# Kernel optimization log

Hardware: AMD Instinct MI355X
Metric: run time of the kernel (lower is better)

The kernel has to match this reference:

```python
import jax, jax.numpy as jnp
import numpy as np

EMBED_DIM = 1408
NUM_HEADS = 16
HEAD_DIM = EMBED_DIM // NUM_HEADS  # 88
SCALE = HEAD_DIM ** -0.5


def setup_inputs() -> dict:
    key = jax.random.key(0)
    k0, k1, k2, k3, k4 = jax.random.split(key, 5)
    B, S, D = 16, 577, EMBED_DIM
    hidden_states = jax.random.normal(k0, (B, S, D), dtype=jnp.float32)
    # fused QKV projection: [D, 3D] laid out as [q | k | v]
    w_qkv = jax.random.normal(k1, (D, 3 * D), dtype=jnp.float32) * (D ** -0.5)
    b_qkv = jax.random.normal(k2, (3 * D,), dtype=jnp.float32) * 0.02
    # output projection
    w_proj = jax.random.normal(k3, (D, D), dtype=jnp.float32) * (D ** -0.5)
    b_proj = jax.random.normal(k4, (D,), dtype=jnp.float32) * 0.02
    return {
        "hidden_states": hidden_states,
        "w_qkv": w_qkv,
        "b_qkv": b_qkv,
        "w_proj": w_proj,
        "b_proj": b_proj,
    }


def reference(hidden_states, w_qkv, b_qkv, w_proj, b_proj):
    B, S, D = hidden_states.shape
    H, Hd = NUM_HEADS, HEAD_DIM
    # fused QKV projection, then chunk along last dim (matches .chunk(3, -1))
    qkv = hidden_states @ w_qkv + b_qkv                      # [B, S, 3D]
    q, k, v = jnp.split(qkv, 3, axis=-1)                     # each [B, S, D]
    q = q.reshape(B, S, H, Hd)
    k = k.reshape(B, S, H, Hd)
    v = v.reshape(B, S, H, Hd)
    # scaled dot-product attention (no mask, no dropout at inference)
    scores = jnp.einsum("bqhd,bkhd->bhqk", q, k) * SCALE      # [B, H, S, S]
    probs = jax.nn.softmax(scores, axis=-1)
    out = jnp.einsum("bhqk,bkhd->bqhd", probs, v)             # [B, S, H, Hd]
    out = out.reshape(B, S, D)
    attn_output = out @ w_proj + b_proj                        # [B, S, D]
    return attn_output
```

## Files before the change

### kernel.cpp

```cpp
#include <hip/hip_runtime.h>
#include <cstddef>
#include <cstdint>

#define D_EMB   1408
#define NHEADS  16
#define HD      88
#define BATCH   16
#define SEQ     577
#define M_ROWS  (BATCH * SEQ)
#define N_QKV   (3 * D_EMB)
#define QKL_N   2816
#define SP      640
#define ATT_SCALE 0.10660035817780521f

#define QT 64
#define KT 64

typedef __attribute__((ext_vector_type(8))) short bf16x8;
typedef __attribute__((ext_vector_type(4))) float f32x4;
typedef unsigned short u16;

static __device__ __forceinline__ u16 f2bf(float x) {
  union { float f; unsigned u; } v; v.f = x;
  unsigned r = v.u + 0x7fff + ((v.u >> 16) & 1);
  return (u16)(r >> 16);
}
static __device__ __forceinline__ float bf2f(u16 h) {
  union { unsigned u; float f; } v; v.u = ((unsigned)h) << 16;
  return v.f;
}
static __device__ __forceinline__ void split_hl(float x, u16* hi, u16* lo) {
  u16 h = f2bf(x);
  *hi = h;
  *lo = f2bf(x - bf2f(h));
}

static __device__ __forceinline__ void async16(const u16* g, u16* l) {
  __builtin_amdgcn_global_load_lds(
      (const __attribute__((address_space(1))) unsigned int*)g,
      (__attribute__((address_space(3))) unsigned int*)l, 16, 0, 0);
}

__global__ __launch_bounds__(256)
void split_kernel(const float* __restrict__ X, u16* __restrict__ H,
                  u16* __restrict__ L, int n4) {
  int i = blockIdx.x * 256 + threadIdx.x;
  if (i >= n4) return;
  float4 v = ((const float4*)X)[i];
  ushort4 h, l;
  split_hl(v.x, &h.x, &l.x);
  split_hl(v.y, &h.y, &l.y);
  split_hl(v.z, &h.z, &l.z);
  split_hl(v.w, &h.w, &l.w);
  ((ushort4*)H)[i] = h;
  ((ushort4*)L)[i] = l;
}

__global__ __launch_bounds__(256)
void transpose_split_kernel(const float* __restrict__ W, u16* __restrict__ Th,
                            u16* __restrict__ Tl, int K, int N) {
  __shared__ float tile[32][33];
  const int n0 = blockIdx.x * 32, k0 = blockIdx.y * 32;
  const int tx = threadIdx.x & 31, ty = threadIdx.x >> 5;
#pragma unroll
  for (int i = 0; i < 4; ++i) {
    int k = ty + i * 8;
    tile[k][tx] = W[(size_t)(k0 + k) * N + n0 + tx];
  }
  __syncthreads();
#pragma unroll
  for (int i = 0; i < 4; ++i) {
    int n = ty + i * 8;
    float v = tile[tx][n];
    u16 h, l;
    split_hl(v, &h, &l);
    Th[(size_t)(n0 + n) * K + k0 + tx] = h;
    Tl[(size_t)(n0 + n) * K + k0 + tx] = l;
  }
}

__global__ __launch_bounds__(256)
void vtrans_kernel(const u16* __restrict__ qkvh, u16* __restrict__ vt) {
  __shared__ u16 tile[64][96];
  const int st = blockIdx.x, bh = blockIdx.y;
  const int b = bh >> 4, h = bh & 15;
  const int tid = threadIdx.x;
  const int s0 = st * 64;
  for (int idx = tid; idx < 64 * 22; idx += 256) {
    int j = idx / 22, c4 = (idx % 22) * 4;
    int s = s0 + j;
    ushort4 v = make_ushort4(0, 0, 0, 0);
    if (s < SEQ)
      v = *(const ushort4*)(qkvh + (size_t)(b * SEQ + s) * N_QKV + 2 * D_EMB + h * HD + c4);
    *(ushort4*)&tile[j][c4] = v;
  }
  if (tid < 64) {
    bf16x8 z = {0, 0, 0, 0, 0, 0, 0, 0};
    *(bf16x8*)&tile[tid][88] = z;
  }
  __syncthreads();
  for (int idx = tid; idx < 96 * 8; idx += 256) {
    int d = idx >> 3, c8 = (idx & 7) * 8;
    bf16x8 o;
#pragma unroll
    for (int e = 0; e < 8; ++e) o[e] = (short)tile[c8 + e][d];
    *(bf16x8*)(vt + ((size_t)bh * 96 + d) * SP + s0 + c8) = o;
  }
}

template <int MODE>
__global__ __launch_bounds__(256)
void gemm3p_kernel(const u16* __restrict__ Ah, const u16* __restrict__ Al,
                   const u16* __restrict__ Bh, const u16* __restrict__ Bl,
                   const float* __restrict__ bias,
                   float* __restrict__ Cf, u16* __restrict__ Ch, u16* __restrict__ Cl,
                   int M, int N, int K, int NX) {
  const int lin  = blockIdx.x;
  const int xcd  = lin & 7;
  const int t    = lin >> 3;
  const int band = xcd + 8 * (t / NX);
  const int nblk = t % NX;
  const int bm0  = band * 128;
  if (bm0 >= M) return;
  const int bn0  = nblk * 128;

  __shared__ u16 sA[2][128 * 32];
  __shared__ u16 sB[2][128 * 32];
  const int tid  = threadIdx.x;
  const int lane = tid & 63;
  const int w    = tid >> 6;
  const int quad = lane >> 4, lc = lane & 15;
  const int wm = w >> 1, wn = w & 1;

  f32x4 acc[4][4];
#pragma unroll
  for (int i = 0; i < 4; ++i)
#pragma unroll
    for (int j = 0; j < 4; ++j) acc[i][j] = (f32x4){0.f, 0.f, 0.f, 0.f};

  for (int k0 = 0; k0 < K; k0 += 32) {
    __syncthreads();
#pragma unroll
    for (int i = 0; i < 2; ++i) {
      int e0  = w * 1024 + i * 512 + lane * 8;
      int r   = e0 >> 5;
      int qp  = (e0 >> 3) & 3;
      int qlg = qp ^ (r & 3);
      int ra  = bm0 + r; if (ra > M - 1) ra = M - 1;
      size_t ga = (size_t)ra * K + (k0 + qlg * 8);
      async16(Ah + ga, &sA[0][w * 1024 + i * 512]);
      async16(Al + ga, &sA[1][w * 1024 + i * 512]);
      size_t gb = (size_t)(bn0 + r) * K + (k0 + qlg * 8);
      async16(Bh + gb, &sB[0][w * 1024 + i * 512]);
      async16(Bl + gb, &sB[1][w * 1024 + i * 512]);
    }
    __syncthreads();

    bf16x8 fah[4], fal[4], fbh[4], fbl[4];
    const int qp = quad ^ (lc & 3);
#pragma unroll
    for (int i = 0; i < 4; ++i) {
      int rowa = wm * 64 + i * 16 + lc;
      fah[i] = *(const bf16x8*)&sA[0][rowa * 32 + qp * 8];
      fal[i] = *(const bf16x8*)&sA[1][rowa * 32 + qp * 8];
      int rowb = wn * 64 + i * 16 + lc;
      fbh[i] = *(const bf16x8*)&sB[0][rowb * 32 + qp * 8];
      fbl[i] = *(const bf16x8*)&sB[1][rowb * 32 + qp * 8];
    }
#pragma unroll
    for (int i = 0; i < 4; ++i)
#pragma unroll
      for (int j = 0; j < 4; ++j) {
        acc[i][j] = __builtin_amdgcn_mfma_f32_16x16x32_bf16(fah[i], fbh[j], acc[i][j], 0, 0, 0);
        acc[i][j] = __builtin_amdgcn_mfma_f32_16x16x32_bf16(fah[i], fbl[j], acc[i][j], 0, 0, 0);
        acc[i][j] = __builtin_amdgcn_mfma_f32_16x16x32_bf16(fal[i], fbh[j], acc[i][j], 0, 0, 0);
      }
  }

#pragma unroll
  for (int j = 0; j < 4; ++j) {
    int col = bn0 + wn * 64 + j * 16 + lc;
    float bj = bias[col];
#pragma unroll
    for (int i = 0; i < 4; ++i) {
#pragma unroll
      for (int rg = 0; rg < 4; ++rg) {
        int row = bm0 + wm * 64 + i * 16 + quad * 4 + rg;
        if (row < M) {
          float v = acc[i][j][rg] + bj;
          if (MODE == 0) {
            Cf[(size_t)row * N + col] = v;
          } else {
            u16 hh, ll;
            split_hl(v, &hh, &ll);
            Ch[(size_t)row * N + col] = hh;
            if (col < QKL_N) Cl[(size_t)row * QKL_N + col] = ll;
          }
        }
      }
    }
  }
}

__global__ __launch_bounds__(256)
void attn_kernel2(const u16* __restrict__ qkvh, const u16* __restrict__ qkvl,
                  const u16* __restrict__ vt,
                  u16* __restrict__ outh, u16* __restrict__ outl) {
  __shared__ u16 Khi[KT][104];
  __shared__ u16 Klo[KT][104];
  __shared__ u16 Vs[96][72];
  __shared__ u16 Pb[QT][72];

  const int tid  = threadIdx.x;
  const int lane = tid & 63;
  const int wv   = tid >> 6;
  const int quad = lane >> 4;
  const int lc   = lane & 15;

  const int qt = blockIdx.x, h = blockIdx.y, b = blockIdx.z;
  const int q0 = qt * QT;

  if (tid < KT) {
    bf16x8 z = {0, 0, 0, 0, 0, 0, 0, 0};
    *(bf16x8*)&Khi[tid][88] = z;
    *(bf16x8*)&Klo[tid][88] = z;
  }

  bf16x8 qh[3], ql[3];
  {
    const bf16x8 z = {0, 0, 0, 0, 0, 0, 0, 0};
    int qrow = q0 + wv * 16 + lc;
    bool qv = qrow < SEQ;
    size_t bh_ = (size_t)(b * SEQ + (qv ? qrow : 0));
#pragma unroll
    for (int ks = 0; ks < 3; ++ks) {
      if (!qv || (ks == 2 && quad == 3)) {
        qh[ks] = z; ql[ks] = z;
      } else {
        qh[ks] = *(const bf16x8*)(qkvh + bh_ * N_QKV + h * HD + ks * 32 + quad * 8);
        ql[ks] = *(const bf16x8*)(qkvl + bh_ * QKL_N + h * HD + ks * 32 + quad * 8);
      }
    }
  }

  float mrow[4], lrow[4];
#pragma unroll
  for (int r = 0; r < 4; ++r) { mrow[r] = -INFINITY; lrow[r] = 0.f; }
  f32x4 oacc[6];
#pragma unroll
  for (int nn = 0; nn < 6; ++nn) oacc[nn] = (f32x4){0.f, 0.f, 0.f, 0.f};

  const u16* vsrc = vt + (size_t)(b * 16 + h) * 96 * SP;

  for (int kt = 0; kt < SP / KT; ++kt) {
    const int k0 = kt * KT;
    __syncthreads();

    for (int idx = tid; idx < KT * 22; idx += 256) {
      int j = idx / 22, c4 = (idx % 22) * 4;
      int s = k0 + j;
      ushort4 kh = make_ushort4(0, 0, 0, 0), kl = make_ushort4(0, 0, 0, 0);
      if (s < SEQ) {
        size_t rb = (size_t)(b * SEQ + s);
        kh = *(const ushort4*)(qkvh + rb * N_QKV + D_EMB + h * HD + c4);
        kl = *(const ushort4*)(qkvl + rb * QKL_N + D_EMB + h * HD + c4);
      }
      *(ushort4*)&Khi[j][c4] = kh;
      *(ushort4*)&Klo[j][c4] = kl;
    }
    for (int idx = tid; idx < 96 * 8; idx += 256) {
      int d = idx >> 3, c8 = (idx & 7) * 8;
      *(bf16x8*)&Vs[d][c8] = *(const bf16x8*)(vsrc + (size_t)d * SP + k0 + c8);
    }
    __syncthreads();

    f32x4 sc[4];
#pragma unroll
    for (int t = 0; t < 4; ++t) {
      f32x4 a = (f32x4){0.f, 0.f, 0.f, 0.f};
#pragma unroll
      for (int ks = 0; ks < 3; ++ks) {
        bf16x8 kh = *(const bf16x8*)&Khi[t * 16 + lc][ks * 32 + quad * 8];
        bf16x8 kl = *(const bf16x8*)&Klo[t * 16 + lc][ks * 32 + quad * 8];
        a = __builtin_amdgcn_mfma_f32_16x16x32_bf16(qh[ks], kh, a, 0, 0, 0);
        a = __builtin_amdgcn_mfma_f32_16x16x32_bf16(qh[ks], kl, a, 0, 0, 0);
        a = __builtin_amdgcn_mfma_f32_16x16x32_bf16(ql[ks], kh, a, 0, 0, 0);
      }
      sc[t] = a;
    }
#pragma unroll
    for (int t = 0; t < 4; ++t) {
      bool valid = (k0 + t * 16 + lc) < SEQ;
#pragma unroll
      for (int r = 0; r < 4; ++r)
        sc[t][r] = valid ? sc[t][r] * ATT_SCALE : -INFINITY;
    }

    float alpha[4];
#pragma unroll
    for (int r = 0; r < 4; ++r) {
      float v = fmaxf(fmaxf(sc[0][r], sc[1][r]), fmaxf(sc[2][r], sc[3][r]));
      v = fmaxf(v, __shfl_xor(v, 1));
      v = fmaxf(v, __shfl_xor(v, 2));
      v = fmaxf(v, __shfl_xor(v, 4));
      v = fmaxf(v, __shfl_xor(v, 8));
      float mnew = fmaxf(mrow[r], v);
      alpha[r] = expf(mrow[r] - mnew);
      mrow[r] = mnew;
      float s = 0.f;
#pragma unroll
      for (int t = 0; t < 4; ++t) {
        float p = expf(sc[t][r] - mnew);
        sc[t][r] = p;
        s += p;
      }
      s += __shfl_xor(s, 1);
      s += __shfl_xor(s, 2);
      s += __shfl_xor(s, 4);
      s += __shfl_xor(s, 8);
      lrow[r] = lrow[r] * alpha[r] + s;
    }
#pragma unroll
    for (int t = 0; t < 4; ++t)
#pragma unroll
      for (int r = 0; r < 4; ++r)
        Pb[wv * 16 + quad * 4 + r][t * 16 + lc] = f2bf(sc[t][r]);
#pragma unroll
    for (int nn = 0; nn < 6; ++nn)
#pragma unroll
      for (int r = 0; r < 4; ++r) oacc[nn][r] *= alpha[r];
    __syncthreads();

    bf16x8 p0 = *(const bf16x8*)&Pb[wv * 16 + lc][quad * 8];
    bf16x8 p1 = *(const bf16x8*)&Pb[wv * 16 + lc][32 + quad * 8];
#pragma unroll
    for (int nn = 0; nn < 6; ++nn) {
      bf16x8 v0 = *(const bf16x8*)&Vs[nn * 16 + lc][quad * 8];
      bf16x8 v1 = *(const bf16x8*)&Vs[nn * 16 + lc][32 + quad * 8];
      oacc[nn] = __builtin_amdgcn_mfma_f32_16x16x32_bf16(p0, v0, oacc[nn], 0, 0, 0);
      oacc[nn] = __builtin_amdgcn_mfma_f32_16x16x32_bf16(p1, v1, oacc[nn], 0, 0, 0);
    }
  }

#pragma unroll
  for (int r = 0; r < 4; ++r) {
    int s = q0 + wv * 16 + quad * 4 + r;
    if (s < SEQ) {
      float inv = 1.f / lrow[r];
      size_t base = (size_t)(b * SEQ + s) * D_EMB + h * HD;
#pragma unroll
      for (int nn = 0; nn < 6; ++nn) {
        int d = nn * 16 + lc;
        if (d < HD) {
          float v = oacc[nn][r] * inv;
          u16 hh, ll;
          split_hl(v, &hh, &ll);
          outh[base + d] = hh;
          outl[base + d] = ll;
        }
      }
    }
  }
}

extern "C" void kernel_launch(void* const* d_in, const int* in_sizes, int n_in,
                              void* d_out, int out_size, void* d_ws, size_t ws_size,
                              hipStream_t stream) {
  const float* hs    = (const float*)d_in[0];
  const float* wqkv  = (const float*)d_in[1];
  const float* bqkv  = (const float*)d_in[2];
  const float* wproj = (const float*)d_in[3];
  const float* bproj = (const float*)d_in[4];
  float* out = (float*)d_out;

  u16* qkvH = (u16*)d_ws;
  u16* qkvL = qkvH + (size_t)M_ROWS * N_QKV;
  u16* hsH  = qkvL + (size_t)M_ROWS * QKL_N;
  u16* hsL  = hsH + (size_t)M_ROWS * D_EMB;
  u16* vt   = hsL + (size_t)M_ROWS * D_EMB;
  u16* wtH  = vt;
  u16* wtL  = wtH + (size_t)N_QKV * D_EMB;
  u16* attnH = hsH;
  u16* attnL = hsL;

  {
    int n4 = (M_ROWS * D_EMB) / 4;
    split_kernel<<<(n4 + 255) / 256, 256, 0, stream>>>(hs, hsH, hsL, n4);
  }
  {
    dim3 g(N_QKV / 32, D_EMB / 32);
    transpose_split_kernel<<<g, 256, 0, stream>>>(wqkv, wtH, wtL, D_EMB, N_QKV);
  }
  {
    gemm3p_kernel<1><<<33 * 80, 256, 0, stream>>>(hsH, hsL, wtH, wtL, bqkv,
                                                  nullptr, qkvH, qkvL,
                                                  M_ROWS, N_QKV, D_EMB, 33);
  }
  {
    dim3 g(SP / 64, BATCH * NHEADS);
    vtrans_kernel<<<g, 256, 0, stream>>>(qkvH, vt);
  }
  {
    dim3 g(SP / QT, NHEADS, BATCH);
    attn_kernel2<<<g, 256, 0, stream>>>(qkvH, qkvL, vt, attnH, attnL);
  }
  {
    dim3 g(D_EMB / 32, D_EMB / 32);
    transpose_split_kernel<<<g, 256, 0, stream>>>(wproj, wtH, wtL, D_EMB, D_EMB);
  }
  {
    gemm3p_kernel<0><<<11 * 80, 256, 0, stream>>>(attnH, attnL, wtH, wtL, bproj,
                                                  out, nullptr, nullptr,
                                                  M_ROWS, D_EMB, D_EMB, 11);
  }
}
```

Before: 949.8 us.

## Rewrite split-bf16 GEMM with 256x128 tiles and triple-buffered async LDS pipeline

Replaces the 128x128, 256-thread split-precision GEMM with a 512-thread kernel using 256x128 output tiles. Global-to-LDS async copies are prefetched two K-steps ahead into three LDS slots, with explicit vmcnt waits, barriers and raised scheduling priority around the MFMA block. The LDS swizzle changes to use row>>1 bits, and K is hard-coded to 1408. The goal is to overlap memory loads with MFMA work and cut sync overhead. The cost is about 147KB of LDS per block, which limits occupancy, and a kernel that is specialised to this K.

```diff
diff --git a/kernel.cpp b/kernel.cpp
--- a/kernel.cpp
+++ b/kernel.cpp
@@ -108,29 +108,104 @@
   }
 }
 
+#define KDIM   1408
+#define BMT    256
+#define BNT    128
+#define SLOT_E 24576
+#define AS_H   0
+#define AS_L   8192
+#define BS_H   16384
+#define BS_L   20480
+
+#define STAGE(SLOTP, SSN)                                                 \
+  {                                                                       \
+    const int k0s = (SSN) * 32;                                           \
+    u16* Ls = &Lds[SLOTP][0];                                             \
+    async16(Ah + srcA0 + k0s, Ls + AS_H + ldsA0);                         \
+    async16(Ah + srcA1 + k0s, Ls + AS_H + ldsA1);                         \
+    async16(Al + srcA0 + k0s, Ls + AS_L + ldsA0);                         \
+    async16(Al + srcA1 + k0s, Ls + AS_L + ldsA1);                         \
+    async16(Bh + srcB0 + k0s, Ls + BS_H + ldsB0);                         \
+    async16(Bl + srcB0 + k0s, Ls + BS_L + ldsB0);                         \
+  }
+
+#define PHASE(SLOT, NXSLOT, SSN, DO_STAGE, VM)                            \
+  {                                                                       \
+    const u16* Lb = &Lds[SLOT][0];                                        \
+    bf16x8 fah[4], fal[4], fbh[4], fbl[4];                                \
+    _Pragma("unroll")                                                     \
+    for (int i = 0; i < 4; ++i) {                                         \
+      fah[i] = *(const bf16x8*)&Lb[AS_H + offA[i]];                       \
+      fal[i] = *(const bf16x8*)&Lb[AS_L + offA[i]];                       \
+      fbh[i] = *(const bf16x8*)&Lb[BS_H + offB[i]];                       \
+      fbl[i] = *(const bf16x8*)&Lb[BS_L + offB[i]];                       \
+    }                                                                     \
+    if (DO_STAGE) STAGE(NXSLOT, SSN);                                     \
+    asm volatile("s_waitcnt vmcnt(" #VM ")" ::: "memory");                \
+    __builtin_amdgcn_s_barrier();                                         \
+    asm volatile("s_waitcnt lgkmcnt(0)" ::: "memory");                    \
+    __builtin_amdgcn_sched_barrier(0);                                    \
+    __builtin_amdgcn_s_setprio(1);                                        \
+    _Pragma("unroll")                                                     \
+    for (int i = 0; i < 4; ++i) {                                         \
+      _Pragma("unroll")                                                   \
+      for (int j = 0; j < 4; ++j) {                                       \
+        acc[i][j] = __builtin_amdgcn_mfma_f32_16x16x32_bf16(fah[i], fbh[j], acc[i][j], 0, 0, 0); \
+        acc[i][j] = __builtin_amdgcn_mfma_f32_16x16x32_bf16(fah[i], fbl[j], acc[i][j], 0, 0, 0); \
+        acc[i][j] = __builtin_amdgcn_mfma_f32_16x16x32_bf16(fal[i], fbh[j], acc[i][j], 0, 0, 0); \
+      }                                                                   \
+    }                                                                     \
+    __builtin_amdgcn_s_setprio(0);                                        \
+    __builtin_amdgcn_s_barrier();                                         \
+  }
+
 template <int MODE>
-__global__ __launch_bounds__(256)
-void gemm3p_kernel(const u16* __restrict__ Ah, const u16* __restrict__ Al,
+__global__ __launch_bounds__(512)
+void gemm8p_kernel(const u16* __restrict__ Ah, const u16* __restrict__ Al,
                    const u16* __restrict__ Bh, const u16* __restrict__ Bl,
                    const float* __restrict__ bias,
                    float* __restrict__ Cf, u16* __restrict__ Ch, u16* __restrict__ Cl,
-                   int M, int N, int K, int NX) {
+                   int M, int N, int NX) {
   const int lin  = blockIdx.x;
   const int xcd  = lin & 7;
   const int t    = lin >> 3;
   const int band = xcd + 8 * (t / NX);
-  const int nblk = t % NX;
-  const int bm0  = band * 128;
+  const int bm0  = band * BMT;
   if (bm0 >= M) return;
-  const int bn0  = nblk * 128;
-
-  __shared__ u16 sA[2][128 * 32];
-  __shared__ u16 sB[2][128 * 32];
+  const int bn0  = (t % NX) * BNT;
+
+  __shared__ u16 Lds[3][SLOT_E];
+
   const int tid  = threadIdx.x;
   const int lane = tid & 63;
   const int w    = tid >> 6;
   const int quad = lane >> 4, lc = lane & 15;
-  const int wm = w >> 1, wn = w & 1;
+  const int wm   = w >> 1, wn = w & 1;
+
+  size_t srcA0, srcA1, srcB0;
+  int ldsA0, ldsA1, ldsB0;
+  {
+    int r0 = tid >> 2, q0 = tid & 3;
+    int ra0 = bm0 + r0; if (ra0 > M - 1) ra0 = M - 1;
+    srcA0 = (size_t)ra0 * KDIM + (size_t)((q0 ^ ((r0 >> 1) & 3)) * 8);
+    ldsA0 = w * 512;
+    int r1 = 128 + r0;
+    int ra1 = bm0 + r1; if (ra1 > M - 1) ra1 = M - 1;
+    srcA1 = (size_t)ra1 * KDIM + (size_t)((q0 ^ ((r1 >> 1) & 3)) * 8);
+    ldsA1 = 4096 + w * 512;
+    srcB0 = (size_t)(bn0 + r0) * KDIM + (size_t)((q0 ^ ((r0 >> 1) & 3)) * 8);
+    ldsB0 = w * 512;
+  }
+
+  int offA[4], offB[4];
+  {
+    const int qphys = quad ^ ((lc >> 1) & 3);
+#pragma unroll
+    for (int i = 0; i < 4; ++i) {
+      offA[i] = (wm * 64 + i * 16 + lc) * 32 + qphys * 8;
+      offB[i] = (wn * 64 + i * 16 + lc) * 32 + qphys * 8;
+    }
+  }
 
   f32x4 acc[4][4];
 #pragma unroll
@@ -138,44 +213,20 @@
 #pragma unroll
     for (int j = 0; j < 4; ++j) acc[i][j] = (f32x4){0.f, 0.f, 0.f, 0.f};
 
-  for (int k0 = 0; k0 < K; k0 += 32) {
-    __syncthreads();
-#pragma unroll
-    for (int i = 0; i < 2; ++i) {
-      int e0  = w * 1024 + i * 512 + lane * 8;
-      int r   = e0 >> 5;
-      int qp  = (e0 >> 3) & 3;
-      int qlg = qp ^ (r & 3);
-      int ra  = bm0 + r; if (ra > M - 1) ra = M - 1;
-      size_t ga = (size_t)ra * K + (k0 + qlg * 8);
-      async16(Ah + ga, &sA[0][w * 1024 + i * 512]);
-      async16(Al + ga, &sA[1][w * 1024 + i * 512]);
-      size_t gb = (size_t)(bn0 + r) * K + (k0 + qlg * 8);
-      async16(Bh + gb, &sB[0][w * 1024 + i * 512]);
-      async16(Bl + gb, &sB[1][w * 1024 + i * 512]);
-    }
-    __syncthreads();
-
-    bf16x8 fah[4], fal[4], fbh[4], fbl[4];
-    const int qp = quad ^ (lc & 3);
-#pragma unroll
-    for (int i = 0; i < 4; ++i) {
-      int rowa = wm * 64 + i * 16 + lc;
-      fah[i] = *(const bf16x8*)&sA[0][rowa * 32 + qp * 8];
-      fal[i] = *(const bf16x8*)&sA[1][rowa * 32 + qp * 8];
-      int rowb = wn * 64 + i * 16 + lc;
-      fbh[i] = *(const bf16x8*)&sB[0][rowb * 32 + qp * 8];
-      fbl[i] = *(const bf16x8*)&sB[1][rowb * 32 + qp * 8];
-    }
-#pragma unroll
-    for (int i = 0; i < 4; ++i)
-#pragma unroll
-      for (int j = 0; j < 4; ++j) {
-        acc[i][j] = __builtin_amdgcn_mfma_f32_16x16x32_bf16(fah[i], fbh[j], acc[i][j], 0, 0, 0);
-        acc[i][j] = __builtin_amdgcn_mfma_f32_16x16x32_bf16(fah[i], fbl[j], acc[i][j], 0, 0, 0);
-        acc[i][j] = __builtin_amdgcn_mfma_f32_16x16x32_bf16(fal[i], fbh[j], acc[i][j], 0, 0, 0);
-      }
-  }
+  STAGE(0, 0);
+  STAGE(1, 1);
+  asm volatile("s_waitcnt vmcnt(6)" ::: "memory");
+  __builtin_amdgcn_s_barrier();
+
+#pragma unroll 1
+  for (int u = 0; u < 14; ++u) {
+    const int s = u * 3;
+    PHASE(0, 2, s + 2, true, 6);
+    PHASE(1, 0, s + 3, true, 6);
+    PHASE(2, 1, s + 4, true, 6);
+  }
+  PHASE(0, 0, 0, false, 0);
+  PHASE(1, 0, 0, false, 0);
 
 #pragma unroll
   for (int j = 0; j < 4; ++j) {
@@ -392,9 +443,9 @@
     transpose_split_kernel<<<g, 256, 0, stream>>>(wqkv, wtH, wtL, D_EMB, N_QKV);
   }
   {
-    gemm3p_kernel<1><<<33 * 80, 256, 0, stream>>>(hsH, hsL, wtH, wtL, bqkv,
+    gemm8p_kernel<1><<<33 * 40, 512, 0, stream>>>(hsH, hsL, wtH, wtL, bqkv,
                                                   nullptr, qkvH, qkvL,
-                                                  M_ROWS, N_QKV, D_EMB, 33);
+                                                  M_ROWS, N_QKV, 33);
   }
   {
     dim3 g(SP / 64, BATCH * NHEADS);
@@ -409,8 +460,8 @@
     transpose_split_kernel<<<g, 256, 0, stream>>>(wproj, wtH, wtL, D_EMB, D_EMB);
   }
   {
-    gemm3p_kernel<0><<<11 * 80, 256, 0, stream>>>(attnH, attnL, wtH, wtL, bproj,
+    gemm8p_kernel<0><<<11 * 40, 512, 0, stream>>>(attnH, attnL, wtH, wtL, bproj,
                                                   out, nullptr, nullptr,
-                                                  M_ROWS, D_EMB, D_EMB, 11);
-  }
-}
+                                                  M_ROWS, D_EMB, 11);
+  }
+}
```

After: 925.3 us. 1.03x faster.
